# Kernel tuning notes

Hardware: AMD Instinct MI355X
Metric: run time of the kernel (lower is better)

## Reference

```python
import jax, jax.numpy as jnp
import numpy as np


def setup_inputs() -> dict:
    key = jax.random.key(0)
    B, N = 32, 262144
    z = jax.random.uniform(key, (B, N, 3), dtype=jnp.float32)
    return {"z": z}


def reference(z):
    # order == 'xyz': lexicographic sort of the N points by (x, y, z),
    # x most significant. jnp.lexsort treats the LAST key as primary,
    # so pass (z_key, y_key, x_key). Sorts along axis=-1 (points),
    # batched over B for free.
    keys = (z[:, :, 2], z[:, :, 1], z[:, :, 0])  # each [B, N]
    idx_pa = jnp.lexsort(keys, axis=-1)          # [B, N] permutation: sorted -> original
    # Original computes torch.sort(gather(arange, idx_pa))[1], which is the
    # inverse permutation of idx_pa; argsort of a permutation inverts it.
    idx_re = jnp.argsort(idx_pa, axis=-1)        # [B, N] original -> sorted position
    return idx_pa, idx_re
```

## Files before the change

kernel.cpp:

```cpp
#include <hip/hip_runtime.h>
#include <stdint.h>

typedef unsigned int u32;
typedef unsigned long long u64;
typedef unsigned char u8;

#define BROWS 32
#define NPTS  262144
#define LOG_NPTS 18
#define CB 256
#define RCAP 1280
#define ROWSTRIDE_FIX (CB * RCAP)
#define CCAP 1536
#define FB2 1024

#define MCH 4096
#define MWG 1024
#define TCH 8192
#define TWG 1024

__device__ __forceinline__ u32 g18_of(float z0) {
    int b = (int)(z0 * 262144.0f);
    return (u32)(b < 0 ? 0 : (b > 262143 ? 262143 : b));
}

__global__ __launch_bounds__(256) void hist_kernel(const float* __restrict__ z,
                                                   u32* __restrict__ counts) {
    __shared__ u32 h[CB];
    for (int i = threadIdx.x; i < CB; i += 256) h[i] = 0;
    __syncthreads();
    int r = blockIdx.x >> 6;
    int c = blockIdx.x & 63;
    size_t base = ((size_t)r << LOG_NPTS) + (size_t)c * 4096;
    for (int k = 0; k < 16; ++k) {
        float z0 = z[(base + (size_t)(k * 256 + threadIdx.x)) * 3];
        atomicAdd(&h[g18_of(z0) >> 10], 1u);
    }
    __syncthreads();
    for (int i = threadIdx.x; i < CB; i += 256)
        if (h[i]) atomicAdd(&counts[r * CB + i], h[i]);
}

__global__ __launch_bounds__(256) void scan_dense(const u32* __restrict__ counts,
                                                  u32* __restrict__ offsets,
                                                  u32* __restrict__ gcur) {
    int r = blockIdx.x, t = threadIdx.x;
    __shared__ u32 sc[CB];
    u32 v = counts[r * CB + t];
    sc[t] = v;
    __syncthreads();
    u32 own = v;
    for (int off = 1; off < CB; off <<= 1) {
        u32 a = (t >= off) ? sc[t - off] : 0;
        __syncthreads();
        sc[t] += a;
        __syncthreads();
    }
    u32 ex = sc[t] - own;
    offsets[r * CB + t] = ex;
    gcur[r * CB + t] = ex;
}

__global__ void init_fixed(u32* __restrict__ gcur) {
    int i = blockIdx.x * 256 + threadIdx.x;
    gcur[i] = (u32)(i & 255) * RCAP;
}

__global__ __launch_bounds__(256) void scan_fixed(const u32* __restrict__ gcur,
                                                  u32* __restrict__ offsets,
                                                  u32* __restrict__ counts) {
    int r = blockIdx.x, t = threadIdx.x;
    __shared__ u32 sc[CB];
    u32 cnt = gcur[r * CB + t] - (u32)t * RCAP;
    if (cnt > RCAP) cnt = RCAP;
    counts[r * CB + t] = cnt;
    sc[t] = cnt;
    __syncthreads();
    u32 own = cnt;
    for (int off = 1; off < CB; off <<= 1) {
        u32 a = (t >= off) ? sc[t - off] : 0;
        __syncthreads();
        sc[t] += a;
        __syncthreads();
    }
    offsets[r * CB + t] = sc[t] - own;
}

__global__ __launch_bounds__(MWG) void ms_scatter(const float* __restrict__ z,
                                                  u32* __restrict__ gcur,
                                                  ulonglong2* __restrict__ recKV,
                                                  int fixedMode) {
    __shared__ u32 h[CB], sc[CB], gb[CB], wtot[4];
    __shared__ ulonglong2 rKV[MCH];
    int t = threadIdx.x;
    int r = blockIdx.x >> 6;
    int c = blockIdx.x & 63;
    if (t < CB) h[t] = 0;
    __syncthreads();
    u64 mh[4], ml[4];
    u32 mpk[4];
    size_t zbase = (((size_t)r << LOG_NPTS) + (size_t)c * MCH) * 3;
#pragma unroll
    for (int k = 0; k < 4; ++k) {
        u32 i = (u32)(c * MCH + k * MWG + t);
        const float* p = z + zbase + (size_t)(k * MWG + t) * 3;
        float f0 = p[0], f1 = p[1], f2 = p[2];
        u32 k0 = __float_as_uint(f0), k1 = __float_as_uint(f1), k2 = __float_as_uint(f2);
        mh[k] = ((u64)k0 << 32) | k1;
        ml[k] = ((u64)k2 << 32) | i;
        u32 b = g18_of(f0) >> 10;
        u32 arr = atomicAdd(&h[b], 1u);
        mpk[k] = (b << 16) | arr;
    }
    __syncthreads();
    u32 scan_s = 0, scan_v = 0;
    int lane = t & 63, wv = t >> 6;
    if (t < CB) {
        scan_v = h[t];
        scan_s = scan_v;
        for (int off = 1; off < 64; off <<= 1) {
            u32 o = __shfl_up(scan_s, off, 64);
            if (lane >= off) scan_s += o;
        }
        if (lane == 63) wtot[wv] = scan_s;
    }
    __syncthreads();
    if (t < CB) {
        u32 wbase = 0;
        if (wv > 0) wbase += wtot[0];
        if (wv > 1) wbase += wtot[1];
        if (wv > 2) wbase += wtot[2];
        sc[t] = wbase + scan_s - scan_v;
        gb[t] = atomicAdd(&gcur[r * CB + t], h[t]);
    }
    __syncthreads();
#pragma unroll
    for (int k = 0; k < 4; ++k) {
        u32 b = mpk[k] >> 16, arr = mpk[k] & 0xFFFFu;
        u32 p = sc[b] + arr;
        rKV[p].x = mh[k];
        rKV[p].y = ml[k];
    }
    __syncthreads();
    size_t rowrec = fixedMode ? (size_t)r * ROWSTRIDE_FIX : ((size_t)r << LOG_NPTS);
#pragma unroll
    for (int k = 0; k < 4; ++k) {
        u32 s = (u32)(k * MWG + t);
        ulonglong2 v = rKV[s];
        u32 b = g18_of(__uint_as_float((u32)(v.x >> 32))) >> 10;
        u32 local = s - sc[b];
        u32 dst = gb[b] + local;
        if (!fixedMode || dst < b * (u32)RCAP + (u32)RCAP)
            recKV[rowrec + dst] = v;
    }
}

__global__ __launch_bounds__(256) void fine_sort(const ulonglong2* __restrict__ recKV,
                                                 const u32* __restrict__ offsets,
                                                 const u32* __restrict__ counts,
                                                 int* __restrict__ out_pa,
                                                 int fixedMode) {
    __shared__ ulonglong2 kv2[CCAP];
    __shared__ u32 fh[FB2], fex[FB2], wtot[4];
    int t = threadIdx.x;
    int g = blockIdx.x;
    int r = g >> 8;
    int cbk = g & 255;
    size_t rowrec = fixedMode ? (size_t)r * ROWSTRIDE_FIX : ((size_t)r << LOG_NPTS);
    u32 rdstart = fixedMode ? (u32)cbk * RCAP : offsets[g];
    u32 wrstart = offsets[g];
    u32 count = counts[g];
    u32 cap = fixedMode ? (u32)RCAP : (u32)CCAP;
    if (count > cap) count = cap;
    for (int i = t; i < FB2; i += 256) fh[i] = 0;
    __syncthreads();

    u64 rh[6], rl[6];
    u32 rpk[6];
#pragma unroll
    for (int k = 0; k < 6; ++k) {
        u32 s = (u32)t + (u32)k * 256u;
        rpk[k] = 0xFFFFFFFFu;
        if (s < count) {
            ulonglong2 rec = recKV[rowrec + rdstart + s];
            rh[k] = rec.x; rl[k] = rec.y;
            u32 fb = g18_of(__uint_as_float((u32)(rec.x >> 32))) & (FB2 - 1);
            u32 arr = atomicAdd(&fh[fb], 1u);
            rpk[k] = (fb << 16) | arr;
        }
    }
    __syncthreads();
    {
        u32 v0 = fh[4 * t], v1 = fh[4 * t + 1], v2 = fh[4 * t + 2], v3 = fh[4 * t + 3];
        u32 tsum = v0 + v1 + v2 + v3;
        u32 s = tsum;
        int lane = t & 63, w = t >> 6;
        for (int off = 1; off < 64; off <<= 1) {
            u32 o = __shfl_up(s, off, 64);
            if (lane >= off) s += o;
        }
        if (lane == 63) wtot[w] = s;
        __syncthreads();
        u32 wbase = 0;
        if (w > 0) wbase += wtot[0];
        if (w > 1) wbase += wtot[1];
        if (w > 2) wbase += wtot[2];
        u32 ex = wbase + s - tsum;
        fex[4 * t] = ex;
        fex[4 * t + 1] = ex + v0;
        fex[4 * t + 2] = ex + v0 + v1;
        fex[4 * t + 3] = ex + v0 + v1 + v2;
    }
    __syncthreads();
#pragma unroll
    for (int k = 0; k < 6; ++k) {
        if (rpk[k] != 0xFFFFFFFFu) {
            u32 fb = rpk[k] >> 16, arr = rpk[k] & 0xFFFFu;
            u32 p = fex[fb] + arr;
            kv2[p].x = rh[k];
            kv2[p].y = rl[k];
        }
    }
    __syncthreads();

    size_t orow = (size_t)r << LOG_NPTS;
#pragma unroll
    for (int k = 0; k < 6; ++k) {
        if (rpk[k] == 0xFFFFFFFFu) continue;
        u32 fb = rpk[k] >> 16;
        u32 cnt = fh[fb];
        u32 rank = 0;
        if (cnt > 1) {
            u32 base = fex[fb];
            for (u32 j = 0; j < cnt; ++j) {
                ulonglong2 b2 = kv2[base + j];
                rank += (b2.x < rh[k]) || (b2.x == rh[k] && b2.y < rl[k]);
            }
        }
        u32 pos = fex[fb] + rank;
        out_pa[orow + wrstart + pos] = (int)(u32)(rl[k] & 0x3FFFFu);
    }
}

__global__ __launch_bounds__(TWG) void trans_ms(const int* __restrict__ out_pa,
                                                u32* __restrict__ tcur,
                                                u32* __restrict__ pairs) {
    __shared__ u32 h[CB], sc[CB], gb[CB], wtot[4];
    __shared__ u32 reord[TCH];
    __shared__ u8 rb8[TCH];
    int t = threadIdx.x;
    int r = blockIdx.x >> 5;
    int c = blockIdx.x & 31;
    if (t < CB) h[t] = 0;
    __syncthreads();
    u32 mpk[8], mv[8];
#pragma unroll
    for (int k = 0; k < 8; ++k) {
        u32 p = (u32)(c * TCH + k * TWG + t);
        u32 si = (u32)out_pa[((size_t)r << LOG_NPTS) + p];
        u32 b = si >> 10;
        mv[k] = ((si & 1023u) << 18) | p;
        u32 arr = atomicAdd(&h[b], 1u);
        mpk[k] = (b << 16) | arr;
    }
    __syncthreads();
    u32 scan_s = 0, scan_v = 0;
    int lane = t & 63, wv = t >> 6;
    if (t < CB) {
        scan_v = h[t];
        scan_s = scan_v;
        for (int off = 1; off < 64; off <<= 1) {
            u32 o = __shfl_up(scan_s, off, 64);
            if (lane >= off) scan_s += o;
        }
        if (lane == 63) wtot[wv] = scan_s;
    }
    __syncthreads();
    if (t < CB) {
        u32 wbase = 0;
        if (wv > 0) wbase += wtot[0];
        if (wv > 1) wbase += wtot[1];
        if (wv > 2) wbase += wtot[2];
        sc[t] = wbase + scan_s - scan_v;
        gb[t] = atomicAdd(&tcur[r * CB + t], h[t]);
    }
    __syncthreads();
#pragma unroll
    for (int k = 0; k < 8; ++k) {
        u32 b = mpk[k] >> 16, arr = mpk[k] & 0xFFFFu;
        u32 p = sc[b] + arr;
        reord[p] = mv[k];
        rb8[p] = (u8)b;
    }
    __syncthreads();
#pragma unroll
    for (int k = 0; k < 8; ++k) {
        u32 s = (u32)(k * TWG + t);
        u32 v = reord[s];
        u32 b = rb8[s];
        u32 local = s - sc[b];
        pairs[((size_t)r << LOG_NPTS) + (size_t)b * 1024 + gb[b] + local] = v;
    }
}

__global__ __launch_bounds__(256) void trans_write(const u32* __restrict__ pairs,
                                                   int* __restrict__ out_re) {
    __shared__ u32 buf[1024];
    int g = blockIdx.x;
    int r = g >> 8, b = g & 255;
    size_t base = ((size_t)r << LOG_NPTS) + (size_t)b * 1024;
#pragma unroll
    for (int k = 0; k < 4; ++k) {
        u32 v = pairs[base + (size_t)(k * 256 + threadIdx.x)];
        buf[v >> 18] = v & 0x3FFFFu;
    }
    __syncthreads();
#pragma unroll
    for (int k = 0; k < 4; ++k) {
        int j = k * 256 + threadIdx.x;
        out_re[base + (size_t)j] = (int)buf[j];
    }
}

extern "C" void kernel_launch(void* const* d_in, const int* in_sizes, int n_in,
                              void* d_out, int out_size, void* d_ws, size_t ws_size,
                              hipStream_t stream) {
    const float* z = (const float*)d_in[0];
    int* out_pa = (int*)d_out;
    int* out_re = out_pa + (size_t)BROWS * NPTS;

    char* ws = (char*)d_ws;
    u32* counts  = (u32*)(ws);
    u32* offsets = (u32*)(ws + (64u << 10));
    u32* gcur    = (u32*)(ws + (128u << 10));
    u32* tcur    = (u32*)(ws + (192u << 10));
    ulonglong2* recKV = (ulonglong2*)(ws + (1u << 20));
    u32* pairs   = (u32*)recKV;

    size_t need = (1ull << 20) + (size_t)BROWS * CB * RCAP * sizeof(ulonglong2);
    int fixedMode = (ws_size >= need) ? 1 : 0;

    hipMemsetAsync(tcur, 0, (size_t)BROWS * CB * sizeof(u32), stream);
    if (fixedMode) {
        init_fixed<<<BROWS, 256, 0, stream>>>(gcur);
        ms_scatter<<<BROWS * 64, MWG, 0, stream>>>(z, gcur, recKV, 1);
        scan_fixed<<<BROWS, 256, 0, stream>>>(gcur, offsets, counts);
        fine_sort<<<BROWS * CB, 256, 0, stream>>>(recKV, offsets, counts, out_pa, 1);
    } else {
        hipMemsetAsync(counts, 0, (size_t)BROWS * CB * sizeof(u32), stream);
        hist_kernel<<<BROWS * 64, 256, 0, stream>>>(z, counts);
        scan_dense<<<BROWS, 256, 0, stream>>>(counts, offsets, gcur);
        ms_scatter<<<BROWS * 64, MWG, 0, stream>>>(z, gcur, recKV, 0);
        fine_sort<<<BROWS * CB, 256, 0, stream>>>(recKV, offsets, counts, out_pa, 0);
    }
    trans_ms<<<BROWS * 32, TWG, 0, stream>>>(out_pa, tcur, pairs);
    trans_write<<<BROWS * CB, 256, 0, stream>>>(pairs, out_re);
}
```

Before: 156.9 us.

## Split sort records into 8-byte keys and 4-byte ids, vectorize loads

Records shrink from 16 bytes to 8-byte (x,y) keys plus a separate 4-byte index array, and the z coordinate is fetched from global memory only on rare exact x,y ties in the fine sort. The scatter kernel now processes 8192 points per block using contiguous float4 loads, and does two shared-memory reorder passes, one for keys and one for ids. The tcur clear is folded into init_fixed, removing a memset launch. This cuts scatter write and fine-sort read traffic, at the cost of an extra reorder pass and occasional uncoalesced z lookups.

```diff
diff --git a/kernel.cpp b/kernel.cpp
--- a/kernel.cpp
+++ b/kernel.cpp
@@ -14,7 +14,7 @@
 #define CCAP 1536
 #define FB2 1024
 
-#define MCH 4096
+#define MCH 8192
 #define MWG 1024
 #define TCH 8192
 #define TWG 1024
@@ -61,9 +61,10 @@
     gcur[r * CB + t] = ex;
 }
 
-__global__ void init_fixed(u32* __restrict__ gcur) {
+__global__ void init_fixed(u32* __restrict__ gcur, u32* __restrict__ tcur) {
     int i = blockIdx.x * 256 + threadIdx.x;
     gcur[i] = (u32)(i & 255) * RCAP;
+    tcur[i] = 0;
 }
 
 __global__ __launch_bounds__(256) void scan_fixed(const u32* __restrict__ gcur,
@@ -88,26 +89,32 @@
 
 __global__ __launch_bounds__(MWG) void ms_scatter(const float* __restrict__ z,
                                                   u32* __restrict__ gcur,
-                                                  ulonglong2* __restrict__ recKV,
+                                                  u64* __restrict__ recK8,
+                                                  u32* __restrict__ recI4,
                                                   int fixedMode) {
     __shared__ u32 h[CB], sc[CB], gb[CB], wtot[4];
-    __shared__ ulonglong2 rKV[MCH];
+    __shared__ u64 r8[MCH];
     int t = threadIdx.x;
-    int r = blockIdx.x >> 6;
-    int c = blockIdx.x & 63;
+    int r = blockIdx.x >> 5;
+    int c = blockIdx.x & 31;
     if (t < CB) h[t] = 0;
     __syncthreads();
-    u64 mh[4], ml[4];
-    u32 mpk[4];
-    size_t zbase = (((size_t)r << LOG_NPTS) + (size_t)c * MCH) * 3;
-#pragma unroll
-    for (int k = 0; k < 4; ++k) {
-        u32 i = (u32)(c * MCH + k * MWG + t);
-        const float* p = z + zbase + (size_t)(k * MWG + t) * 3;
-        float f0 = p[0], f1 = p[1], f2 = p[2];
-        u32 k0 = __float_as_uint(f0), k1 = __float_as_uint(f1), k2 = __float_as_uint(f2);
+
+    u32 base_pt = (u32)(c * MCH + t * 8);
+    const float4* zf4 = (const float4*)(z + ((size_t)r << LOG_NPTS) * 3 + (size_t)base_pt * 3);
+    float4 f[6];
+#pragma unroll
+    for (int j = 0; j < 6; ++j) f[j] = zf4[j];
+    const float* ff = (const float*)f;
+
+    u64 mh[8];
+    u32 mi[8], mpk[8];
+#pragma unroll
+    for (int k = 0; k < 8; ++k) {
+        float f0 = ff[3 * k], f1 = ff[3 * k + 1];
+        u32 k0 = __float_as_uint(f0), k1 = __float_as_uint(f1);
         mh[k] = ((u64)k0 << 32) | k1;
-        ml[k] = ((u64)k2 << 32) | i;
+        mi[k] = base_pt + (u32)k;
         u32 b = g18_of(f0) >> 10;
         u32 arr = atomicAdd(&h[b], 1u);
         mpk[k] = (b << 16) | arr;
@@ -126,41 +133,61 @@
     }
     __syncthreads();
     if (t < CB) {
-        u32 wbase = 0;
-        if (wv > 0) wbase += wtot[0];
-        if (wv > 1) wbase += wtot[1];
-        if (wv > 2) wbase += wtot[2];
-        sc[t] = wbase + scan_s - scan_v;
+        u32 wb = 0;
+        if (wv > 0) wb += wtot[0];
+        if (wv > 1) wb += wtot[1];
+        if (wv > 2) wb += wtot[2];
+        sc[t] = wb + scan_s - scan_v;
         gb[t] = atomicAdd(&gcur[r * CB + t], h[t]);
     }
     __syncthreads();
-#pragma unroll
-    for (int k = 0; k < 4; ++k) {
+    size_t rowrec = fixedMode ? (size_t)r * ROWSTRIDE_FIX : ((size_t)r << LOG_NPTS);
+
+#pragma unroll
+    for (int k = 0; k < 8; ++k) {
         u32 b = mpk[k] >> 16, arr = mpk[k] & 0xFFFFu;
-        u32 p = sc[b] + arr;
-        rKV[p].x = mh[k];
-        rKV[p].y = ml[k];
-    }
-    __syncthreads();
-    size_t rowrec = fixedMode ? (size_t)r * ROWSTRIDE_FIX : ((size_t)r << LOG_NPTS);
-#pragma unroll
-    for (int k = 0; k < 4; ++k) {
+        r8[sc[b] + arr] = mh[k];
+    }
+    __syncthreads();
+#pragma unroll
+    for (int k = 0; k < 8; ++k) {
         u32 s = (u32)(k * MWG + t);
-        ulonglong2 v = rKV[s];
-        u32 b = g18_of(__uint_as_float((u32)(v.x >> 32))) >> 10;
+        u64 v = r8[s];
+        u32 b = g18_of(__uint_as_float((u32)(v >> 32))) >> 10;
         u32 local = s - sc[b];
         u32 dst = gb[b] + local;
-        if (!fixedMode || dst < b * (u32)RCAP + (u32)RCAP)
-            recKV[rowrec + dst] = v;
-    }
-}
-
-__global__ __launch_bounds__(256) void fine_sort(const ulonglong2* __restrict__ recKV,
+        if (!fixedMode || dst < (b + 1u) * (u32)RCAP)
+            recK8[rowrec + dst] = v;
+    }
+    __syncthreads();
+    u32* ri = (u32*)r8;
+#pragma unroll
+    for (int k = 0; k < 8; ++k) {
+        u32 b = mpk[k] >> 16, arr = mpk[k] & 0xFFFFu;
+        ri[sc[b] + arr] = (b << 18) | mi[k];
+    }
+    __syncthreads();
+#pragma unroll
+    for (int k = 0; k < 8; ++k) {
+        u32 s = (u32)(k * MWG + t);
+        u32 v = ri[s];
+        u32 b = v >> 18;
+        u32 local = s - sc[b];
+        u32 dst = gb[b] + local;
+        if (!fixedMode || dst < (b + 1u) * (u32)RCAP)
+            recI4[rowrec + dst] = v & 0x3FFFFu;
+    }
+}
+
+__global__ __launch_bounds__(256) void fine_sort(const u64* __restrict__ recK8,
+                                                 const u32* __restrict__ recI4,
+                                                 const float* __restrict__ z,
                                                  const u32* __restrict__ offsets,
                                                  const u32* __restrict__ counts,
                                                  int* __restrict__ out_pa,
                                                  int fixedMode) {
-    __shared__ ulonglong2 kv2[CCAP];
+    __shared__ u64 k8[CCAP];
+    __shared__ u32 ki[CCAP];
     __shared__ u32 fh[FB2], fex[FB2], wtot[4];
     int t = threadIdx.x;
     int g = blockIdx.x;
@@ -175,16 +202,17 @@
     for (int i = t; i < FB2; i += 256) fh[i] = 0;
     __syncthreads();
 
-    u64 rh[6], rl[6];
-    u32 rpk[6];
+    u64 rh[6];
+    u32 rid[6], rpk[6];
 #pragma unroll
     for (int k = 0; k < 6; ++k) {
         u32 s = (u32)t + (u32)k * 256u;
         rpk[k] = 0xFFFFFFFFu;
         if (s < count) {
-            ulonglong2 rec = recKV[rowrec + rdstart + s];
-            rh[k] = rec.x; rl[k] = rec.y;
-            u32 fb = g18_of(__uint_as_float((u32)(rec.x >> 32))) & (FB2 - 1);
+            u64 hi = recK8[rowrec + rdstart + s];
+            u32 id = recI4[rowrec + rdstart + s];
+            rh[k] = hi; rid[k] = id;
+            u32 fb = g18_of(__uint_as_float((u32)(hi >> 32))) & (FB2 - 1);
             u32 arr = atomicAdd(&fh[fb], 1u);
             rpk[k] = (fb << 16) | arr;
         }
@@ -217,13 +245,14 @@
         if (rpk[k] != 0xFFFFFFFFu) {
             u32 fb = rpk[k] >> 16, arr = rpk[k] & 0xFFFFu;
             u32 p = fex[fb] + arr;
-            kv2[p].x = rh[k];
-            kv2[p].y = rl[k];
+            k8[p] = rh[k];
+            ki[p] = rid[k];
         }
     }
     __syncthreads();
 
     size_t orow = (size_t)r << LOG_NPTS;
+    size_t zrow = ((size_t)r << LOG_NPTS) * 3;
 #pragma unroll
     for (int k = 0; k < 6; ++k) {
         if (rpk[k] == 0xFFFFFFFFu) continue;
@@ -232,13 +261,23 @@
         u32 rank = 0;
         if (cnt > 1) {
             u32 base = fex[fb];
+            u64 e8 = rh[k];
+            u32 ei = rid[k];
             for (u32 j = 0; j < cnt; ++j) {
-                ulonglong2 b2 = kv2[base + j];
-                rank += (b2.x < rh[k]) || (b2.x == rh[k] && b2.y < rl[k]);
+                u64 b8 = k8[base + j];
+                if (b8 < e8) { ++rank; continue; }
+                if (b8 == e8) {
+                    u32 bi = ki[base + j];
+                    if (bi != ei) {
+                        u32 bk2 = __float_as_uint(z[zrow + (size_t)bi * 3 + 2]);
+                        u32 ek2 = __float_as_uint(z[zrow + (size_t)ei * 3 + 2]);
+                        rank += (bk2 < ek2) || (bk2 == ek2 && bi < ei);
+                    }
+                }
             }
         }
         u32 pos = fex[fb] + rank;
-        out_pa[orow + wrstart + pos] = (int)(u32)(rl[k] & 0x3FFFFu);
+        out_pa[orow + wrstart + pos] = (int)rid[k];
     }
 }
 
@@ -334,24 +373,25 @@
     u32* offsets = (u32*)(ws + (64u << 10));
     u32* gcur    = (u32*)(ws + (128u << 10));
     u32* tcur    = (u32*)(ws + (192u << 10));
-    ulonglong2* recKV = (ulonglong2*)(ws + (1u << 20));
-    u32* pairs   = (u32*)recKV;
-
-    size_t need = (1ull << 20) + (size_t)BROWS * CB * RCAP * sizeof(ulonglong2);
+    u64* recK8   = (u64*)(ws + (1u << 20));
+    u32* recI4   = (u32*)(ws + (1u << 20) + (80ull << 20));
+    u32* pairs   = (u32*)recK8;
+
+    size_t need = (1ull << 20) + (121ull << 20);
     int fixedMode = (ws_size >= need) ? 1 : 0;
 
-    hipMemsetAsync(tcur, 0, (size_t)BROWS * CB * sizeof(u32), stream);
     if (fixedMode) {
-        init_fixed<<<BROWS, 256, 0, stream>>>(gcur);
-        ms_scatter<<<BROWS * 64, MWG, 0, stream>>>(z, gcur, recKV, 1);
+        init_fixed<<<BROWS, 256, 0, stream>>>(gcur, tcur);
+        ms_scatter<<<BROWS * 32, MWG, 0, stream>>>(z, gcur, recK8, recI4, 1);
         scan_fixed<<<BROWS, 256, 0, stream>>>(gcur, offsets, counts);
-        fine_sort<<<BROWS * CB, 256, 0, stream>>>(recKV, offsets, counts, out_pa, 1);
+        fine_sort<<<BROWS * CB, 256, 0, stream>>>(recK8, recI4, z, offsets, counts, out_pa, 1);
     } else {
         hipMemsetAsync(counts, 0, (size_t)BROWS * CB * sizeof(u32), stream);
+        hipMemsetAsync(tcur, 0, (size_t)BROWS * CB * sizeof(u32), stream);
         hist_kernel<<<BROWS * 64, 256, 0, stream>>>(z, counts);
         scan_dense<<<BROWS, 256, 0, stream>>>(counts, offsets, gcur);
-        ms_scatter<<<BROWS * 64, MWG, 0, stream>>>(z, gcur, recKV, 0);
-        fine_sort<<<BROWS * CB, 256, 0, stream>>>(recKV, offsets, counts, out_pa, 0);
+        ms_scatter<<<BROWS * 32, MWG, 0, stream>>>(z, gcur, recK8, recI4, 0);
+        fine_sort<<<BROWS * CB, 256, 0, stream>>>(recK8, recI4, z, offsets, counts, out_pa, 0);
     }
     trans_ms<<<BROWS * 32, TWG, 0, stream>>>(out_pa, tcur, pairs);
     trans_write<<<BROWS * CB, 256, 0, stream>>>(pairs, out_re);
```

Result: faster. 141.1 us (-10.1%).
